# Kernel optimization log

Hardware: AMD Instinct MI355X
Metric: run time of the kernel (lower is better)

## Reference

```python
import jax, jax.numpy as jnp
import numpy as np

N_NODES = 100000
N_EDGES = 1600000
IN_DIM, HIDDEN, OUT_DIM = 128, 64, 32


def setup_inputs() -> dict:
    key = jax.random.key(0)
    k1, k2, k3, k4 = jax.random.split(key, 4)
    x = jax.random.normal(k1, (N_NODES, IN_DIM), dtype=jnp.float32)
    # Glorot-style init for the two GCN linear layers
    W1 = jax.random.normal(k2, (IN_DIM, HIDDEN), dtype=jnp.float32) * (1.0 / np.sqrt(IN_DIM))
    b1 = jnp.zeros((HIDDEN,), dtype=jnp.float32)
    W2 = jax.random.normal(k3, (HIDDEN, OUT_DIM), dtype=jnp.float32) * (1.0 / np.sqrt(HIDDEN))
    b2 = jnp.zeros((OUT_DIM,), dtype=jnp.float32)
    edge_index = jax.random.randint(k4, (2, N_EDGES), 0, N_NODES, dtype=jnp.int32)
    return {"x": x, "W1": W1, "b1": b1, "W2": W2, "b2": b2, "edge_index": edge_index}


def _gcn_norm(edge_index, n_nodes):
    # Add self-loops and compute symmetric normalization D^{-1/2} (A+I) D^{-1/2}
    loops = jnp.arange(n_nodes, dtype=edge_index.dtype)
    src = jnp.concatenate([edge_index[0], loops])  # [E+N]
    dst = jnp.concatenate([edge_index[1], loops])
    deg = jax.ops.segment_sum(jnp.ones_like(dst, dtype=jnp.float32), dst,
                              num_segments=n_nodes)
    dinv = jnp.where(deg > 0, jax.lax.rsqrt(deg), 0.0)
    norm = dinv[src] * dinv[dst]  # [E+N]
    return src, dst, norm


def _gcn_conv(h, W, b, src, dst, norm, n_nodes):
    h = h @ W                                   # [N, out] linear transform first
    msg = h[src] * norm[:, None]                # gather + per-edge scale
    agg = jax.ops.segment_sum(msg, dst, num_segments=n_nodes)  # scatter-add
    return agg + b


def reference(x, W1, b1, W2, b2, edge_index):
    n = x.shape[0]
    src, dst, norm = _gcn_norm(edge_index, n)
    h = jax.nn.relu(_gcn_conv(x, W1, b1, src, dst, norm, n))
    # dropout is identity in eval mode (deterministic reference)
    z = _gcn_conv(h, W2, b2, src, dst, norm, n)
    return z
```

## Files before the change

kernel.cpp:

```cpp
#include <hip/hip_runtime.h>
#include <hip/hip_fp16.h>

#define NB_MAX 784
#define CAP    2560
#define CHUNK  8192

typedef _Float16 half8 __attribute__((ext_vector_type(8)));
typedef float f32x4_t __attribute__((ext_vector_type(4)));

__global__ __launch_bounds__(256) void k_bin(const int* __restrict__ src,
                                             const int* __restrict__ dst,
                                             int* __restrict__ gcur,
                                             int* __restrict__ binned,
                                             int nb, int e) {
    __shared__ int hist[NB_MAX];
    __shared__ int curs[NB_MAX];
    const int t = threadIdx.x;
    const int base = blockIdx.x * CHUNK;
    const int lim = min(CHUNK, e - base);

    for (int i = t; i < NB_MAX; i += 256) hist[i] = 0;
    __syncthreads();

    const int i4lim = lim >> 2;
    for (int i = t; i < i4lim; i += 256) {
        int4 d = ((const int4*)(dst + base))[i];
        atomicAdd(&hist[d.x >> 7], 1);
        atomicAdd(&hist[d.y >> 7], 1);
        atomicAdd(&hist[d.z >> 7], 1);
        atomicAdd(&hist[d.w >> 7], 1);
    }
    for (int i = (i4lim << 2) + t; i < lim; i += 256)
        atomicAdd(&hist[dst[base + i] >> 7], 1);
    __syncthreads();

    for (int b = t; b < nb; b += 256) {
        int h = hist[b];
        curs[b] = h ? atomicAdd(&gcur[b], h) : 0;
    }
    __syncthreads();

    for (int i = t; i < i4lim; i += 256) {
        int4 d = ((const int4*)(dst + base))[i];
        int4 s = ((const int4*)(src + base))[i];
        int o0 = atomicAdd(&curs[d.x >> 7], 1);
        int o1 = atomicAdd(&curs[d.y >> 7], 1);
        int o2 = atomicAdd(&curs[d.z >> 7], 1);
        int o3 = atomicAdd(&curs[d.w >> 7], 1);
        if (o0 < CAP) binned[(size_t)(d.x >> 7) * CAP + o0] = (s.x << 7) | (d.x & 127);
        if (o1 < CAP) binned[(size_t)(d.y >> 7) * CAP + o1] = (s.y << 7) | (d.y & 127);
        if (o2 < CAP) binned[(size_t)(d.z >> 7) * CAP + o2] = (s.z << 7) | (d.z & 127);
        if (o3 < CAP) binned[(size_t)(d.w >> 7) * CAP + o3] = (s.w << 7) | (d.w & 127);
    }
    for (int i = (i4lim << 2) + t; i < lim; i += 256) {
        int d = dst[base + i], s = src[base + i];
        int off = atomicAdd(&curs[d >> 7], 1);
        if (off < CAP) binned[(size_t)(d >> 7) * CAP + off] = (s << 7) | (d & 127);
    }
}

__global__ __launch_bounds__(1024) void k_base(const int* __restrict__ gcur,
                                               int* __restrict__ cbase,
                                               int* __restrict__ rpx,
                                               int nb, int n, int e) {
    __shared__ int sm[1024];
    int t = threadIdx.x;
    int v = (t < nb) ? gcur[t] : 0;
    sm[t] = v;
    __syncthreads();
    for (int o = 1; o < 1024; o <<= 1) {
        int add = (t >= o) ? sm[t - o] : 0;
        __syncthreads();
        sm[t] += add;
        __syncthreads();
    }
    if (t < nb) cbase[t] = sm[t] - v;
    if (t == 0) rpx[n] = e;
}

__global__ __launch_bounds__(256) void k_sort(const int* __restrict__ binned,
                                              const int* __restrict__ gcur,
                                              const int* __restrict__ cbase,
                                              int* __restrict__ csr,
                                              int* __restrict__ rpx,
                                              float* __restrict__ dinv, int n) {
    __shared__ int hist[128], offs[128];
    const int t = threadIdx.x;
    const int b = blockIdx.x;
    if (t < 128) hist[t] = 0;
    __syncthreads();

    int sz = gcur[b];
    if (sz > CAP) sz = CAP;
    const int* bp = binned + (size_t)b * CAP;

    const int i4 = sz >> 2;
    for (int i = t; i < i4; i += 256) {
        int4 p = ((const int4*)bp)[i];
        atomicAdd(&hist[p.x & 127], 1);
        atomicAdd(&hist[p.y & 127], 1);
        atomicAdd(&hist[p.z & 127], 1);
        atomicAdd(&hist[p.w & 127], 1);
    }
    for (int i = (i4 << 2) + t; i < sz; i += 256)
        atomicAdd(&hist[bp[i] & 127], 1);
    __syncthreads();

    if (t < 128) offs[t] = hist[t];
    __syncthreads();
    for (int o = 1; o < 128; o <<= 1) {
        int add = (t < 128 && t >= o) ? offs[t - o] : 0;
        __syncthreads();
        if (t < 128) offs[t] += add;
        __syncthreads();
    }

    const int base = cbase[b];
    if (t < 128) {
        int node = (b << 7) + t;
        if (node < n) {
            rpx[node]  = base + offs[t] - hist[t];
            dinv[node] = rsqrtf(1.0f + (float)hist[t]);
        }
    }
    __syncthreads();
    if (t < 128) hist[t] = offs[t] - hist[t];
    __syncthreads();

    for (int i = t; i < sz; i += 256) {
        int p = bp[i];
        int pos = base + atomicAdd(&hist[p & 127], 1);
        csr[pos] = p >> 7;
    }
}

__global__ __launch_bounds__(256) void k_gemm1(const float* __restrict__ x,
                                               const float* __restrict__ W1,
                                               const float* __restrict__ dinv,
                                               __half* __restrict__ hp, int n) {
    __shared__ _Float16 wt[64 * 136];
    const int t = threadIdx.x;

    for (int i = t; i < 128 * 64; i += 256) {
        int k = i >> 6, o = i & 63;
        wt[o * 136 + k] = (_Float16)W1[i];
    }
    __syncthreads();

    const int lane = t & 63;
    const int wid  = t >> 6;
    const int row0 = blockIdx.x * 64 + wid * 16;
    const int rA   = lane & 15;
    const int g    = lane >> 4;

    f32x4_t acc0 = {0.f, 0.f, 0.f, 0.f};
    f32x4_t acc1 = {0.f, 0.f, 0.f, 0.f};
    f32x4_t acc2 = {0.f, 0.f, 0.f, 0.f};
    f32x4_t acc3 = {0.f, 0.f, 0.f, 0.f};

    const int arow = min(row0 + rA, n - 1);
    const float* ap0 = x + (size_t)arow * 128 + g * 8;

#pragma unroll
    for (int ks = 0; ks < 4; ++ks) {
        const float* ap = ap0 + ks * 32;
        float4 a0 = *(const float4*)ap;
        float4 a1 = *(const float4*)(ap + 4);
        half8 af;
        af[0] = (_Float16)a0.x; af[1] = (_Float16)a0.y;
        af[2] = (_Float16)a0.z; af[3] = (_Float16)a0.w;
        af[4] = (_Float16)a1.x; af[5] = (_Float16)a1.y;
        af[6] = (_Float16)a1.z; af[7] = (_Float16)a1.w;

        const _Float16* wb = wt + rA * 136 + ks * 32 + g * 8;
        half8 b0 = *(const half8*)(wb);
        half8 b1 = *(const half8*)(wb + 16 * 136);
        half8 b2 = *(const half8*)(wb + 32 * 136);
        half8 b3 = *(const half8*)(wb + 48 * 136);
        acc0 = __builtin_amdgcn_mfma_f32_16x16x32_f16(af, b0, acc0, 0, 0, 0);
        acc1 = __builtin_amdgcn_mfma_f32_16x16x32_f16(af, b1, acc1, 0, 0, 0);
        acc2 = __builtin_amdgcn_mfma_f32_16x16x32_f16(af, b2, acc2, 0, 0, 0);
        acc3 = __builtin_amdgcn_mfma_f32_16x16x32_f16(af, b3, acc3, 0, 0, 0);
    }

    _Float16* hph = (_Float16*)hp;
#pragma unroll
    for (int r = 0; r < 4; ++r) {
        int node = row0 + g * 4 + r;
        if (node >= n) continue;
        float di = dinv[node];
        _Float16* o = hph + (size_t)node * 64 + rA;
        o[0]  = (_Float16)(acc0[r] * di);
        o[16] = (_Float16)(acc1[r] * di);
        o[32] = (_Float16)(acc2[r] * di);
        o[48] = (_Float16)(acc3[r] * di);
    }
}


union Pk8 { float4 f4; __half2 h2[4]; };

__device__ inline void addrow(float acc[8], float4 v) {
    Pk8 u; u.f4 = v;
#pragma unroll
    for (int j = 0; j < 4; ++j) {
        float2 t = __half22float2(u.h2[j]);
        acc[2 * j]     += t.x;
        acc[2 * j + 1] += t.y;
    }
}

__global__ __launch_bounds__(256) void k_agg1(const int* __restrict__ rpx,
                                              const int* __restrict__ csr,
                                              const __half* __restrict__ hp,
                                              const float* __restrict__ dinv,
                                              const float* __restrict__ b1,
                                              const float* __restrict__ W2,
                                              __half* __restrict__ hp2, int n) {
    __shared__ float w2t[32 * 68];
    __shared__ float tl[32 * 68];
    const int t = threadIdx.x;

    for (int i = t; i < 64 * 32; i += 256) {
        int f = i >> 5, j = i & 31;
        w2t[j * 68 + f] = W2[i];
    }

    const int nl   = t >> 3;
    const int q    = t & 7;
    const int node = blockIdx.x * 32 + nl;
    const bool alive = node < n;

    float acc[8];
#pragma unroll
    for (int j = 0; j < 8; ++j) acc[j] = 0.f;

    float di = 0.f;
    if (alive) {
        const float4* hp4 = (const float4*)hp;
        int start = rpx[node], end = rpx[node + 1];
        addrow(acc, hp4[(size_t)node * 8 + q]);

        int p = start;
        for (; p + 8 <= end; p += 8) {
            int s[8];
#pragma unroll
            for (int j = 0; j < 8; ++j) s[j] = csr[p + j];
            float4 v[8];
#pragma unroll
            for (int j = 0; j < 8; ++j) v[j] = hp4[(size_t)s[j] * 8 + q];
#pragma unroll
            for (int j = 0; j < 8; ++j) addrow(acc, v[j]);
        }
        for (; p + 2 <= end; p += 2) {
            int s0 = csr[p], s1 = csr[p + 1];
            float4 v0 = hp4[(size_t)s0 * 8 + q];
            float4 v1 = hp4[(size_t)s1 * 8 + q];
            addrow(acc, v0);
            addrow(acc, v1);
        }
        if (p < end)
            addrow(acc, hp4[(size_t)csr[p] * 8 + q]);

        di = dinv[node];
    }

    float4 ba = ((const float4*)b1)[q * 2];
    float4 bb = ((const float4*)b1)[q * 2 + 1];
    float4 t0, t1;
    t0.x = fmaxf(fmaf(acc[0], di, ba.x), 0.f);
    t0.y = fmaxf(fmaf(acc[1], di, ba.y), 0.f);
    t0.z = fmaxf(fmaf(acc[2], di, ba.z), 0.f);
    t0.w = fmaxf(fmaf(acc[3], di, ba.w), 0.f);
    t1.x = fmaxf(fmaf(acc[4], di, bb.x), 0.f);
    t1.y = fmaxf(fmaf(acc[5], di, bb.y), 0.f);
    t1.z = fmaxf(fmaf(acc[6], di, bb.z), 0.f);
    t1.w = fmaxf(fmaf(acc[7], di, bb.w), 0.f);
    *(float4*)(tl + nl * 68 + q * 8)     = t0;
    *(float4*)(tl + nl * 68 + q * 8 + 4) = t1;
    __syncthreads();

    if (!alive) return;

    const float* trow = tl + nl * 68;
    const float* wa = w2t + q * 68;
    const float* wb = w2t + (q + 8) * 68;
    const float* wc = w2t + (q + 16) * 68;
    const float* wd = w2t + (q + 24) * 68;
    float o0 = 0.f, o1 = 0.f, o2 = 0.f, o3 = 0.f;
#pragma unroll
    for (int f4 = 0; f4 < 16; ++f4) {
        float4 tv = *(const float4*)(trow + f4 * 4);
        float4 v0 = *(const float4*)(wa + f4 * 4);
        float4 v1 = *(const float4*)(wb + f4 * 4);
        float4 v2 = *(const float4*)(wc + f4 * 4);
        float4 v3 = *(const float4*)(wd + f4 * 4);
        o0 += tv.x * v0.x + tv.y * v0.y + tv.z * v0.z + tv.w * v0.w;
        o1 += tv.x * v1.x + tv.y * v1.y + tv.z * v1.z + tv.w * v1.w;
        o2 += tv.x * v2.x + tv.y * v2.y + tv.z * v2.z + tv.w * v2.w;
        o3 += tv.x * v3.x + tv.y * v3.y + tv.z * v3.z + tv.w * v3.w;
    }
    _Float16* hq = (_Float16*)hp2 + (size_t)node * 32;
    hq[q]      = (_Float16)(o0 * di);
    hq[q + 8]  = (_Float16)(o1 * di);
    hq[q + 16] = (_Float16)(o2 * di);
    hq[q + 24] = (_Float16)(o3 * di);
}

template<int LOGF>
__global__ __launch_bounds__(256) void k_aggregate(const int* __restrict__ rpx,
                                                   const int* __restrict__ csr,
                                                   const __half* __restrict__ hp,
                                                   const float* __restrict__ dinv,
                                                   const float* __restrict__ bias,
                                                   float* __restrict__ out, int n) {
    constexpr int F   = 1 << LOGF;
    constexpr int TPN = F / 8;
    int gid  = blockIdx.x * 256 + threadIdx.x;
    int node = gid / TPN;
    int q    = gid % TPN;
    if (node >= n) return;

    const float4* hp4 = (const float4*)hp;
    int start = rpx[node], end = rpx[node + 1];

    float acc[8];
#pragma unroll
    for (int j = 0; j < 8; ++j) acc[j] = 0.f;
    addrow(acc, hp4[(size_t)node * TPN + q]);

    int p = start;
    for (; p + 8 <= end; p += 8) {
        int s[8];
#pragma unroll
        for (int j = 0; j < 8; ++j) s[j] = csr[p + j];
        float4 v[8];
#pragma unroll
        for (int j = 0; j < 8; ++j) v[j] = hp4[(size_t)s[j] * TPN + q];
#pragma unroll
        for (int j = 0; j < 8; ++j) addrow(acc, v[j]);
    }
    for (; p + 2 <= end; p += 2) {
        int s0 = csr[p], s1 = csr[p + 1];
        float4 v0 = hp4[(size_t)s0 * TPN + q];
        float4 v1 = hp4[(size_t)s1 * TPN + q];
        addrow(acc, v0);
        addrow(acc, v1);
    }
    if (p < end)
        addrow(acc, hp4[(size_t)csr[p] * TPN + q]);

    float di = dinv[node];
    float4 b0 = ((const float4*)bias)[q * 2];
    float4 b1v = ((const float4*)bias)[q * 2 + 1];
    float4 r0, r1;
    r0.x = fmaf(acc[0], di, b0.x); r0.y = fmaf(acc[1], di, b0.y);
    r0.z = fmaf(acc[2], di, b0.z); r0.w = fmaf(acc[3], di, b0.w);
    r1.x = fmaf(acc[4], di, b1v.x); r1.y = fmaf(acc[5], di, b1v.y);
    r1.z = fmaf(acc[6], di, b1v.z); r1.w = fmaf(acc[7], di, b1v.w);
    float4* o4 = (float4*)out;
    o4[(size_t)node * (F / 4) + q * 2]     = r0;
    o4[(size_t)node * (F / 4) + q * 2 + 1] = r1;
}


extern "C" void kernel_launch(void* const* d_in, const int* in_sizes, int n_in,
                              void* d_out, int out_size, void* d_ws, size_t ws_size,
                              hipStream_t stream) {
    const float* x  = (const float*)d_in[0];
    const float* W1 = (const float*)d_in[1];
    const float* b1 = (const float*)d_in[2];
    const float* W2 = (const float*)d_in[3];
    const float* b2 = (const float*)d_in[4];
    const int*   ei = (const int*)d_in[5];

    const int N = in_sizes[0] / 128;
    const int E = in_sizes[5] / 2;
    const int* src = ei;
    const int* dst = ei + E;
    const int NB = (N + 127) >> 7;

    char* w = (char*)d_ws;
    int*    gcur   = (int*)w;                  w += NB_MAX * 4;
    int*    cbase  = (int*)w;                  w += NB_MAX * 4;
    int*    rpx    = (int*)w;                  w += (size_t)(N + 4) * 4;
    float*  dinv   = (float*)w;                w += (size_t)N * 4;
    int*    binned = (int*)w;                  w += (size_t)NB_MAX * CAP * 4;
    int*    csr    = (int*)w;                  w += (size_t)E * 4;
    __half* hp     = (__half*)w;               w += (size_t)N * 64 * 2;
    __half* hp2    = (__half*)w;               w += (size_t)N * 32 * 2;
    float*  out    = (float*)d_out;

    hipMemsetAsync(gcur, 0, NB_MAX * 4, stream);

    k_bin <<<(E + CHUNK - 1) / CHUNK, 256, 0, stream>>>(src, dst, gcur, binned, NB, E);
    k_base<<<1, 1024, 0, stream>>>(gcur, cbase, rpx, NB, N, E);
    k_sort<<<NB, 256, 0, stream>>>(binned, gcur, cbase, csr, rpx, dinv, N);

    k_gemm1<<<(N + 63) / 64, 256, 0, stream>>>(x, W1, dinv, hp, N);

    k_agg1<<<(N + 31) / 32, 256, 0, stream>>>(rpx, csr, hp, dinv, b1, W2, hp2, N);

    k_aggregate<5><<<(N * 4 + 255) / 256, 256, 0, stream>>>(rpx, csr, hp2, dinv, b2, out, N);
}
```

Baseline: 141.9 us.

## Fuse edge binning with first GEMM and move source-degree scaling into aggregation

The first GEMM no longer depends on dinv, so it is merged into the edge-binning kernel as extra blocks of one launch, letting the dense transform run concurrently with the binning atomics. Source-side normalization moves into agg1, which now gathers dinv[src] per edge and applies it with an FMA. This removes one launch and the serial dependency of the GEMM on the sort, but adds a random 4-byte gather per edge in the aggregation. The merged kernel also shares its LDS buffer between the two roles, sized to the larger one.

New measurement: 136.4 us. 1.04x faster.

```diff
diff --git a/kernel.cpp b/kernel.cpp
--- a/kernel.cpp
+++ b/kernel.cpp
@@ -8,54 +8,115 @@
 typedef _Float16 half8 __attribute__((ext_vector_type(8)));
 typedef float f32x4_t __attribute__((ext_vector_type(4)));
 
-__global__ __launch_bounds__(256) void k_bin(const int* __restrict__ src,
-                                             const int* __restrict__ dst,
-                                             int* __restrict__ gcur,
-                                             int* __restrict__ binned,
-                                             int nb, int e) {
-    __shared__ int hist[NB_MAX];
-    __shared__ int curs[NB_MAX];
+__global__ __launch_bounds__(256) void k_bin_gemm1(
+        const int* __restrict__ src, const int* __restrict__ dst,
+        int* __restrict__ gcur, int* __restrict__ binned, int nb, int e,
+        const float* __restrict__ x, const float* __restrict__ W1,
+        __half* __restrict__ hp, int n, int binb) {
+    __shared__ __align__(16) char smem[64 * 136 * 2];
     const int t = threadIdx.x;
-    const int base = blockIdx.x * CHUNK;
-    const int lim = min(CHUNK, e - base);
-
-    for (int i = t; i < NB_MAX; i += 256) hist[i] = 0;
-    __syncthreads();
-
-    const int i4lim = lim >> 2;
-    for (int i = t; i < i4lim; i += 256) {
-        int4 d = ((const int4*)(dst + base))[i];
-        atomicAdd(&hist[d.x >> 7], 1);
-        atomicAdd(&hist[d.y >> 7], 1);
-        atomicAdd(&hist[d.z >> 7], 1);
-        atomicAdd(&hist[d.w >> 7], 1);
-    }
-    for (int i = (i4lim << 2) + t; i < lim; i += 256)
-        atomicAdd(&hist[dst[base + i] >> 7], 1);
-    __syncthreads();
-
-    for (int b = t; b < nb; b += 256) {
-        int h = hist[b];
-        curs[b] = h ? atomicAdd(&gcur[b], h) : 0;
-    }
-    __syncthreads();
-
-    for (int i = t; i < i4lim; i += 256) {
-        int4 d = ((const int4*)(dst + base))[i];
-        int4 s = ((const int4*)(src + base))[i];
-        int o0 = atomicAdd(&curs[d.x >> 7], 1);
-        int o1 = atomicAdd(&curs[d.y >> 7], 1);
-        int o2 = atomicAdd(&curs[d.z >> 7], 1);
-        int o3 = atomicAdd(&curs[d.w >> 7], 1);
-        if (o0 < CAP) binned[(size_t)(d.x >> 7) * CAP + o0] = (s.x << 7) | (d.x & 127);
-        if (o1 < CAP) binned[(size_t)(d.y >> 7) * CAP + o1] = (s.y << 7) | (d.y & 127);
-        if (o2 < CAP) binned[(size_t)(d.z >> 7) * CAP + o2] = (s.z << 7) | (d.z & 127);
-        if (o3 < CAP) binned[(size_t)(d.w >> 7) * CAP + o3] = (s.w << 7) | (d.w & 127);
-    }
-    for (int i = (i4lim << 2) + t; i < lim; i += 256) {
-        int d = dst[base + i], s = src[base + i];
-        int off = atomicAdd(&curs[d >> 7], 1);
-        if (off < CAP) binned[(size_t)(d >> 7) * CAP + off] = (s << 7) | (d & 127);
+
+    if (blockIdx.x < binb) {
+        int* hist = (int*)smem;
+        int* curs = hist + NB_MAX;
+        const int base = blockIdx.x * CHUNK;
+        const int lim = min(CHUNK, e - base);
+
+        for (int i = t; i < NB_MAX; i += 256) hist[i] = 0;
+        __syncthreads();
+
+        const int i4lim = lim >> 2;
+        for (int i = t; i < i4lim; i += 256) {
+            int4 d = ((const int4*)(dst + base))[i];
+            atomicAdd(&hist[d.x >> 7], 1);
+            atomicAdd(&hist[d.y >> 7], 1);
+            atomicAdd(&hist[d.z >> 7], 1);
+            atomicAdd(&hist[d.w >> 7], 1);
+        }
+        for (int i = (i4lim << 2) + t; i < lim; i += 256)
+            atomicAdd(&hist[dst[base + i] >> 7], 1);
+        __syncthreads();
+
+        for (int b = t; b < nb; b += 256) {
+            int h = hist[b];
+            curs[b] = h ? atomicAdd(&gcur[b], h) : 0;
+        }
+        __syncthreads();
+
+        for (int i = t; i < i4lim; i += 256) {
+            int4 d = ((const int4*)(dst + base))[i];
+            int4 s = ((const int4*)(src + base))[i];
+            int o0 = atomicAdd(&curs[d.x >> 7], 1);
+            int o1 = atomicAdd(&curs[d.y >> 7], 1);
+            int o2 = atomicAdd(&curs[d.z >> 7], 1);
+            int o3 = atomicAdd(&curs[d.w >> 7], 1);
+            if (o0 < CAP) binned[(size_t)(d.x >> 7) * CAP + o0] = (s.x << 7) | (d.x & 127);
+            if (o1 < CAP) binned[(size_t)(d.y >> 7) * CAP + o1] = (s.y << 7) | (d.y & 127);
+            if (o2 < CAP) binned[(size_t)(d.z >> 7) * CAP + o2] = (s.z << 7) | (d.z & 127);
+            if (o3 < CAP) binned[(size_t)(d.w >> 7) * CAP + o3] = (s.w << 7) | (d.w & 127);
+        }
+        for (int i = (i4lim << 2) + t; i < lim; i += 256) {
+            int d = dst[base + i], s = src[base + i];
+            int off = atomicAdd(&curs[d >> 7], 1);
+            if (off < CAP) binned[(size_t)(d >> 7) * CAP + off] = (s << 7) | (d & 127);
+        }
+        return;
+    }
+
+    _Float16* wt = (_Float16*)smem;
+
+    for (int i = t; i < 128 * 64; i += 256) {
+        int k = i >> 6, o = i & 63;
+        wt[o * 136 + k] = (_Float16)W1[i];
+    }
+    __syncthreads();
+
+    const int lane = t & 63;
+    const int wid  = t >> 6;
+    const int row0 = (blockIdx.x - binb) * 64 + wid * 16;
+    const int rA   = lane & 15;
+    const int g    = lane >> 4;
+
+    f32x4_t acc0 = {0.f, 0.f, 0.f, 0.f};
+    f32x4_t acc1 = {0.f, 0.f, 0.f, 0.f};
+    f32x4_t acc2 = {0.f, 0.f, 0.f, 0.f};
+    f32x4_t acc3 = {0.f, 0.f, 0.f, 0.f};
+
+    const int arow = min(row0 + rA, n - 1);
+    const float* ap0 = x + (size_t)arow * 128 + g * 8;
+
+#pragma unroll
+    for (int ks = 0; ks < 4; ++ks) {
+        const float* ap = ap0 + ks * 32;
+        float4 a0 = *(const float4*)ap;
+        float4 a1 = *(const float4*)(ap + 4);
+        half8 af;
+        af[0] = (_Float16)a0.x; af[1] = (_Float16)a0.y;
+        af[2] = (_Float16)a0.z; af[3] = (_Float16)a0.w;
+        af[4] = (_Float16)a1.x; af[5] = (_Float16)a1.y;
+        af[6] = (_Float16)a1.z; af[7] = (_Float16)a1.w;
+
+        const _Float16* wb = wt + rA * 136 + ks * 32 + g * 8;
+        half8 b0 = *(const half8*)(wb);
+        half8 b1 = *(const half8*)(wb + 16 * 136);
+        half8 b2 = *(const half8*)(wb + 32 * 136);
+        half8 b3 = *(const half8*)(wb + 48 * 136);
+        acc0 = __builtin_amdgcn_mfma_f32_16x16x32_f16(af, b0, acc0, 0, 0, 0);
+        acc1 = __builtin_amdgcn_mfma_f32_16x16x32_f16(af, b1, acc1, 0, 0, 0);
+        acc2 = __builtin_amdgcn_mfma_f32_16x16x32_f16(af, b2, acc2, 0, 0, 0);
+        acc3 = __builtin_amdgcn_mfma_f32_16x16x32_f16(af, b3, acc3, 0, 0, 0);
+    }
+
+    _Float16* hph = (_Float16*)hp;
+#pragma unroll
+    for (int r = 0; r < 4; ++r) {
+        int node = row0 + g * 4 + r;
+        if (node >= n) continue;
+        _Float16* o = hph + (size_t)node * 64 + rA;
+        o[0]  = (_Float16)acc0[r];
+        o[16] = (_Float16)acc1[r];
+        o[32] = (_Float16)acc2[r];
+        o[48] = (_Float16)acc3[r];
     }
 }
 
@@ -134,69 +195,6 @@
     }
 }
 
-__global__ __launch_bounds__(256) void k_gemm1(const float* __restrict__ x,
-                                               const float* __restrict__ W1,
-                                               const float* __restrict__ dinv,
-                                               __half* __restrict__ hp, int n) {
-    __shared__ _Float16 wt[64 * 136];
-    const int t = threadIdx.x;
-
-    for (int i = t; i < 128 * 64; i += 256) {
-        int k = i >> 6, o = i & 63;
-        wt[o * 136 + k] = (_Float16)W1[i];
-    }
-    __syncthreads();
-
-    const int lane = t & 63;
-    const int wid  = t >> 6;
-    const int row0 = blockIdx.x * 64 + wid * 16;
-    const int rA   = lane & 15;
-    const int g    = lane >> 4;
-
-    f32x4_t acc0 = {0.f, 0.f, 0.f, 0.f};
-    f32x4_t acc1 = {0.f, 0.f, 0.f, 0.f};
-    f32x4_t acc2 = {0.f, 0.f, 0.f, 0.f};
-    f32x4_t acc3 = {0.f, 0.f, 0.f, 0.f};
-
-    const int arow = min(row0 + rA, n - 1);
-    const float* ap0 = x + (size_t)arow * 128 + g * 8;
-
-#pragma unroll
-    for (int ks = 0; ks < 4; ++ks) {
-        const float* ap = ap0 + ks * 32;
-        float4 a0 = *(const float4*)ap;
-        float4 a1 = *(const float4*)(ap + 4);
-        half8 af;
-        af[0] = (_Float16)a0.x; af[1] = (_Float16)a0.y;
-        af[2] = (_Float16)a0.z; af[3] = (_Float16)a0.w;
-        af[4] = (_Float16)a1.x; af[5] = (_Float16)a1.y;
-        af[6] = (_Float16)a1.z; af[7] = (_Float16)a1.w;
-
-        const _Float16* wb = wt + rA * 136 + ks * 32 + g * 8;
-        half8 b0 = *(const half8*)(wb);
-        half8 b1 = *(const half8*)(wb + 16 * 136);
-        half8 b2 = *(const half8*)(wb + 32 * 136);
-        half8 b3 = *(const half8*)(wb + 48 * 136);
-        acc0 = __builtin_amdgcn_mfma_f32_16x16x32_f16(af, b0, acc0, 0, 0, 0);
-        acc1 = __builtin_amdgcn_mfma_f32_16x16x32_f16(af, b1, acc1, 0, 0, 0);
-        acc2 = __builtin_amdgcn_mfma_f32_16x16x32_f16(af, b2, acc2, 0, 0, 0);
-        acc3 = __builtin_amdgcn_mfma_f32_16x16x32_f16(af, b3, acc3, 0, 0, 0);
-    }
-
-    _Float16* hph = (_Float16*)hp;
-#pragma unroll
-    for (int r = 0; r < 4; ++r) {
-        int node = row0 + g * 4 + r;
-        if (node >= n) continue;
-        float di = dinv[node];
-        _Float16* o = hph + (size_t)node * 64 + rA;
-        o[0]  = (_Float16)(acc0[r] * di);
-        o[16] = (_Float16)(acc1[r] * di);
-        o[32] = (_Float16)(acc2[r] * di);
-        o[48] = (_Float16)(acc3[r] * di);
-    }
-}
-
 
 union Pk8 { float4 f4; __half2 h2[4]; };
 
@@ -207,6 +205,16 @@
         float2 t = __half22float2(u.h2[j]);
         acc[2 * j]     += t.x;
         acc[2 * j + 1] += t.y;
+    }
+}
+
+__device__ inline void addrow_s(float acc[8], float4 v, float s) {
+    Pk8 u; u.f4 = v;
+#pragma unroll
+    for (int j = 0; j < 4; ++j) {
+        float2 t = __half22float2(u.h2[j]);
+        acc[2 * j]     = fmaf(t.x, s, acc[2 * j]);
+        acc[2 * j + 1] = fmaf(t.y, s, acc[2 * j + 1]);
     }
 }
 
@@ -239,30 +247,35 @@
     if (alive) {
         const float4* hp4 = (const float4*)hp;
         int start = rpx[node], end = rpx[node + 1];
-        addrow(acc, hp4[(size_t)node * 8 + q]);
+        di = dinv[node];
+        addrow_s(acc, hp4[(size_t)node * 8 + q], di);
 
         int p = start;
         for (; p + 8 <= end; p += 8) {
             int s[8];
 #pragma unroll
             for (int j = 0; j < 8; ++j) s[j] = csr[p + j];
+            float ds[8];
+#pragma unroll
+            for (int j = 0; j < 8; ++j) ds[j] = dinv[s[j]];
             float4 v[8];
 #pragma unroll
             for (int j = 0; j < 8; ++j) v[j] = hp4[(size_t)s[j] * 8 + q];
 #pragma unroll
-            for (int j = 0; j < 8; ++j) addrow(acc, v[j]);
+            for (int j = 0; j < 8; ++j) addrow_s(acc, v[j], ds[j]);
         }
         for (; p + 2 <= end; p += 2) {
             int s0 = csr[p], s1 = csr[p + 1];
+            float d0 = dinv[s0], d1 = dinv[s1];
             float4 v0 = hp4[(size_t)s0 * 8 + q];
             float4 v1 = hp4[(size_t)s1 * 8 + q];
-            addrow(acc, v0);
-            addrow(acc, v1);
-        }
-        if (p < end)
-            addrow(acc, hp4[(size_t)csr[p] * 8 + q]);
-
-        di = dinv[node];
+            addrow_s(acc, v0, d0);
+            addrow_s(acc, v1, d1);
+        }
+        if (p < end) {
+            int s0 = csr[p];
+            addrow_s(acc, hp4[(size_t)s0 * 8 + q], dinv[s0]);
+        }
     }
 
     float4 ba = ((const float4*)b1)[q * 2];
@@ -391,14 +404,17 @@
     __half* hp2    = (__half*)w;               w += (size_t)N * 32 * 2;
     float*  out    = (float*)d_out;
 
+    const int binb = (E + CHUNK - 1) / CHUNK;
+    const int gb1  = (N + 63) / 64;
+
     hipMemsetAsync(gcur, 0, NB_MAX * 4, stream);
 
-    k_bin <<<(E + CHUNK - 1) / CHUNK, 256, 0, stream>>>(src, dst, gcur, binned, NB, E);
+    k_bin_gemm1<<<binb + gb1, 256, 0, stream>>>(src, dst, gcur, binned, NB, E,
+                                                x, W1, hp, N, binb);
+
     k_base<<<1, 1024, 0, stream>>>(gcur, cbase, rpx, NB, N, E);
     k_sort<<<NB, 256, 0, stream>>>(binned, gcur, cbase, csr, rpx, dinv, N);
 
-    k_gemm1<<<(N + 63) / 64, 256, 0, stream>>>(x, W1, dinv, hp, N);
-
     k_agg1<<<(N + 31) / 32, 256, 0, stream>>>(rpx, csr, hp, dinv, b1, W2, hp2, N);
 
     k_aggregate<5><<<(N * 4 + 255) / 256, 256, 0, stream>>>(rpx, csr, hp2, dinv, b2, out, N);
```
